# Kernel optimization log

Measured on AMD Instinct MI355X. Metric: run time of the kernel, lower is better.

## Reference

```python
import jax, jax.numpy as jnp
import numpy as np

N_NODES = 100000
N_EDGES = 800000
IN_FEATS = 64
H_FEATS = 64
INTER = 64
NUM_CLASSES = 32
NEG_SLOPE = 0.01  # torch leaky_relu default


def setup_inputs() -> dict:
    key = jax.random.key(0)
    ks = jax.random.split(key, 16)
    inp = {
        "gate_type": jax.random.randint(ks[0], (N_NODES,), 0, IN_FEATS),
        "src": jax.random.randint(ks[1], (N_EDGES,), 0, N_NODES),
        "dst": jax.random.randint(ks[2], (N_EDGES,), 0, N_NODES),
        "src_idx": jax.random.uniform(ks[3], (N_EDGES,), dtype=jnp.float32),
        "dst_idx": jax.random.uniform(ks[4], (N_EDGES,), dtype=jnp.float32),
        "rev": jax.random.uniform(ks[5], (N_EDGES,), dtype=jnp.float32),
        "emb": jax.random.normal(ks[6], (IN_FEATS, IN_FEATS), dtype=jnp.float32) * 0.1,
        # 5 stacked QConv layers (in_feats == h_feats so shapes coincide)
        "W1": jax.random.normal(ks[7], (5, INTER, IN_FEATS + 3), dtype=jnp.float32) * 0.1,
        "W2": jax.random.normal(ks[8], (5, H_FEATS, IN_FEATS + INTER), dtype=jnp.float32) * 0.1,
        "b2": jnp.zeros((5, H_FEATS), dtype=jnp.float32),
        "Wl1": jax.random.normal(ks[9], (H_FEATS, H_FEATS), dtype=jnp.float32) * 0.1,
        "bl1": jnp.zeros((H_FEATS,), dtype=jnp.float32),
        "Wl2": jax.random.normal(ks[10], (NUM_CLASSES, H_FEATS), dtype=jnp.float32) * 0.1,
        "bl2": jnp.zeros((NUM_CLASSES,), dtype=jnp.float32),
    }
    return inp


def _leaky_relu(x):
    return jnp.where(x >= 0, x, NEG_SLOPE * x)


def reference(gate_type, src, dst, src_idx, dst_idx, rev,
              emb, W1, W2, b2, Wl1, bl1, Wl2, bl2):
    n = gate_type.shape[0]
    # edge feature w: [E, 3]
    w = jnp.stack([src_idx, dst_idx, rev], axis=1)
    # in-degree for mailbox mean (zero-degree nodes get h_N = 0, as in DGL)
    deg = jax.ops.segment_sum(jnp.ones((src.shape[0],), w.dtype), dst, num_segments=n)
    inv_deg = (1.0 / jnp.maximum(deg, 1.0))[:, None]  # [N, 1]

    h = emb[gate_type]  # [N, F] embedding lookup
    for i in range(5):
        m = jnp.concatenate([h[src], w], axis=1)          # [E, F+3] gather
        tmp = _leaky_relu(m @ W1[i].T)                     # [E, inter]
        h_N = jax.ops.segment_sum(tmp, dst, num_segments=n) * inv_deg  # mean mailbox
        h = jax.nn.relu(jnp.concatenate([h, h_N], axis=1) @ W2[i].T + b2[i])
    h = jax.nn.relu(h @ Wl1.T + bl1)
    return h @ Wl2.T + bl2  # [N, num_classes]
```

## Files before the change

### kernel.cpp

```cpp
#include <hip/hip_runtime.h>

#define NN 100000
#define NE 800000
#define NBUCK 196
#define EPB 3125
#define BCAP 6144

typedef __attribute__((ext_vector_type(8))) short short8;
typedef __attribute__((ext_vector_type(4))) float f32x4;
typedef unsigned long long u64;

__device__ __forceinline__ unsigned short f2b(float x) {
  unsigned int u = __float_as_uint(x);
  u = u + 0x7fffu + ((u >> 16) & 1u);
  return (unsigned short)(u >> 16);
}
__device__ __forceinline__ float b2f(unsigned short s) {
  return __uint_as_float(((unsigned int)s) << 16);
}

__global__ __launch_bounds__(256) void wprep(
    const float* __restrict__ W1, const float* __restrict__ W2,
    const float* __restrict__ Wl1, const float* __restrict__ Wl2,
    unsigned short* __restrict__ w1p, unsigned short* __restrict__ w2p,
    unsigned short* __restrict__ wl1p, unsigned short* __restrict__ wl2p,
    float* __restrict__ wcolp) {
  int i = blockIdx.x * 256 + threadIdx.x;
  if (i < 20480) {
    int l = i >> 12, r = i & 4095, c = r >> 6, k = r & 63;
    int idx = (((c * 64 + k) * 2) ^ ((c & 7) << 4)) >> 1;
    w1p[l * 4096 + idx] = f2b(W1[(l * 64 + c) * 67 + k]);
  } else if (i < 61440) {
    int j = i - 20480;
    int l = j >> 13, r = j & 8191, c = r >> 7, k = r & 127;
    int idx = (((c * 128 + k) * 2) ^ ((c & 7) << 4)) >> 1;
    w2p[l * 8192 + idx] = f2b(W2[(l * 64 + c) * 128 + k]);
  } else if (i < 65536) {
    int j = i - 61440;
    int c = j >> 6, k = j & 63;
    int idx = (((c * 64 + k) * 2) ^ ((c & 7) << 4)) >> 1;
    wl1p[idx] = f2b(Wl1[c * 64 + k]);
  } else if (i < 67584) {
    int j = i - 65536;
    int c = j >> 6, k = j & 63;
    int idx = (((c * 64 + k) * 2) ^ ((c & 7) << 4)) >> 1;
    wl2p[idx] = f2b(Wl2[c * 64 + k]);
  } else if (i < 68544) {
    int j = i - 67584;
    int l = j / 192, r = j % 192, jj = r >> 6, f = r & 63;
    wcolp[(l * 3 + jj) * 64 + f] = W1[(l * 64 + f) * 67 + 64 + jj];
  }
}


__global__ __launch_bounds__(256) void ehist(const int* __restrict__ dst,
                                             int* __restrict__ hp) {
  __shared__ int lh[NBUCK];
  int tid = threadIdx.x;
  if (tid < NBUCK) lh[tid] = 0;
  __syncthreads();
  int e0 = blockIdx.x * EPB;
  for (int i = tid; i < EPB; i += 256) atomicAdd(&lh[dst[e0 + i] >> 9], 1);
  __syncthreads();
  if (tid < NBUCK) hp[blockIdx.x * NBUCK + tid] = lh[tid];
}

__global__ __launch_bounds__(256) void escatter(
    const int* __restrict__ dst, const int* __restrict__ src,
    const float* __restrict__ si, const float* __restrict__ di,
    const float* __restrict__ rv, const int* __restrict__ hp,
    u64* __restrict__ erec_tmp, unsigned short* __restrict__ lbkt) {
  __shared__ int cur[NBUCK];
  __shared__ int wsum[4];
  int tid = threadIdx.x;
  int myblk = blockIdx.x;
  int tot = 0, mypre = 0;
  if (tid < NBUCK) {
    for (int blk = 0; blk < 256; ++blk) {
      int v = hp[blk * NBUCK + tid];
      tot += v;
      if (blk < myblk) mypre += v;
    }
  }
  int lane = tid & 63, wv = tid >> 6;
  int s = tot;
#pragma unroll
  for (int off = 1; off < 64; off <<= 1) {
    int t = __shfl_up(s, off);
    if (lane >= off) s += t;
  }
  if (lane == 63) wsum[wv] = s;
  __syncthreads();
  int wpre = 0;
  for (int j = 0; j < wv; ++j) wpre += wsum[j];
  int excl = s + wpre - tot;
  if (tid < NBUCK) cur[tid] = excl + mypre;
  __syncthreads();
  int e0 = myblk * EPB;
  for (int i = tid; i < EPB; i += 256) {
    int e = e0 + i;
    int d = dst[e];
    int pos = atomicAdd(&cur[d >> 9], 1);
    unsigned int a = (unsigned int)fminf(si[e] * 32768.f, 32767.f);
    unsigned int b = (unsigned int)fminf(di[e] * 32768.f, 32767.f);
    unsigned int c = (unsigned int)fminf(rv[e] * 32768.f, 32767.f);
    u64 u = (u64)(src[e] & 0x1FFFF) | ((u64)a << 17) | ((u64)b << 32) |
            ((u64)c << 47);
    erec_tmp[pos] = u;
    lbkt[pos] = (unsigned short)(d & 511);
  }
}

__global__ __launch_bounds__(256) void bucket_csr(
    const unsigned short* __restrict__ lbkt, const int* __restrict__ hp,
    const u64* __restrict__ erec_tmp, u64* __restrict__ erec,
    int* __restrict__ deg, float4* __restrict__ meta, int* __restrict__ nhp) {
  __shared__ unsigned short lb[BCAP];
  __shared__ int cnt[512];
  __shared__ int excl[512];
  __shared__ int dh[64];
  __shared__ int wsum[4];
  __shared__ int btot[NBUCK];
  __shared__ int bexcl[NBUCK];
  int b = blockIdx.x, tid = threadIdx.x;
  int tot = 0;
  if (tid < NBUCK) {
    for (int blk = 0; blk < 256; ++blk) tot += hp[blk * NBUCK + tid];
    btot[tid] = tot;
  }
  int lane = tid & 63, wv = tid >> 6;
  int s = tot;
#pragma unroll
  for (int off = 1; off < 64; off <<= 1) {
    int t = __shfl_up(s, off);
    if (lane >= off) s += t;
  }
  if (lane == 63) wsum[wv] = s;
  __syncthreads();
  int wpre = 0;
  for (int j = 0; j < wv; ++j) wpre += wsum[j];
  if (tid < NBUCK) bexcl[tid] = s + wpre - tot;
  cnt[2 * tid] = 0;
  cnt[2 * tid + 1] = 0;
  if (tid < 64) dh[tid] = 0;
  __syncthreads();
  int s0 = bexcl[b];
  int size = btot[b];
  if (size > BCAP) size = BCAP;
  for (int p = tid; p < size; p += 256) {
    unsigned short v = lbkt[s0 + p];
    lb[p] = v;
    atomicAdd(&cnt[v], 1);
  }
  __syncthreads();
  int a = cnt[2 * tid], c = cnt[2 * tid + 1];
  int ps = a + c;
  int v2 = ps;
#pragma unroll
  for (int off = 1; off < 64; off <<= 1) {
    int t = __shfl_up(v2, off);
    if (lane >= off) v2 += t;
  }
  __syncthreads();
  if (lane == 63) wsum[wv] = v2;
  __syncthreads();
  int wpre2 = 0;
  for (int j = 0; j < wv; ++j) wpre2 += wsum[j];
  int ex = v2 + wpre2 - ps;
  excl[2 * tid] = ex;
  excl[2 * tid + 1] = ex + a;
  int n0 = b << 9;
#pragma unroll
  for (int j = 0; j < 2; ++j) {
    int i = 2 * tid + j;
    int n = n0 + i;
    if (n < NN) {
      int d = j ? c : a;
      int rs = s0 + (j ? ex + a : ex);
      deg[n] = d;
      float4 m;
      m.x = __int_as_float(rs);
      m.y = __int_as_float(d);
      m.z = 1.0f / (float)((d > 1) ? d : 1);
      m.w = 0.f;
      meta[n] = m;
      atomicAdd(&dh[(d < 63) ? d : 63], 1);
    }
  }
  cnt[2 * tid] = 0;
  cnt[2 * tid + 1] = 0;
  __syncthreads();
  for (int p = tid; p < size; p += 256) {
    int ld = lb[p];
    int pos = excl[ld] + atomicAdd(&cnt[ld], 1);
    erec[s0 + pos] = erec_tmp[s0 + p];
  }
  if (tid < 64) nhp[b * 64 + tid] = dh[tid];
}

__global__ __launch_bounds__(256) void nscatter(
    const int* __restrict__ deg, const int* __restrict__ nhp,
    int* __restrict__ order) {
  __shared__ int cur[64];
  int tid = threadIdx.x;
  int myblk = blockIdx.x;
  if (tid < 64) {
    int tot = 0, mypre = 0;
    for (int blk = 0; blk < NBUCK; ++blk) {
      int v = nhp[blk * 64 + tid];
      tot += v;
      if (blk < myblk) mypre += v;
    }
    int s = tot;
#pragma unroll
    for (int off = 1; off < 64; off <<= 1) {
      int t = __shfl_up(s, off);
      if (tid >= off) s += t;
    }
    cur[tid] = (s - tot) + mypre;
  }
  __syncthreads();
  int n0 = myblk * 512;
#pragma unroll
  for (int j = 0; j < 2; ++j) {
    int n = n0 + tid + j * 256;
    if (n < NN) {
      int d = deg[n];
      int pos = atomicAdd(&cur[(d < 63) ? d : 63], 1);
      order[pos] = n;
    }
  }
}


__global__ __launch_bounds__(256) void aggregate(
    const unsigned short* __restrict__ H1, const float4* __restrict__ meta,
    const int* __restrict__ order, const u64* __restrict__ erec,
    const float* __restrict__ wcolp, unsigned short* __restrict__ hNs) {
  __shared__ float wcol[3][64];
  int tid = threadIdx.x;
  if (tid < 192) ((float*)wcol)[tid] = wcolp[tid];
  __syncthreads();
  int l = tid & 63;
  int fl = l & 15, f0 = fl * 4;
  int qidx = blockIdx.x * 16 + (tid >> 4);
  float wa[4], wb[4], wc[4];
#pragma unroll
  for (int j = 0; j < 4; ++j) {
    wa[j] = wcol[0][f0 + j];
    wb[j] = wcol[1][f0 + j];
    wc[j] = wcol[2][f0 + j];
  }
  if (qidx >= NN) return;
  int n = order[qidx];
  float4 m = meta[n];
  int s0 = __float_as_int(m.x);
  int cnt = __float_as_int(m.y);
  float invd = m.z;
  float acc[4] = {0.f, 0.f, 0.f, 0.f};
  u64 r0 = 0, r1 = 0, r2 = 0;
  ushort4 h0 = make_ushort4(0, 0, 0, 0), h1 = h0;
  if (cnt > 0) {
    r0 = erec[s0];
    h0 = *(const ushort4*)&H1[(size_t)(r0 & 0x1FFFF) * 64 + f0];
  }
  if (cnt > 1) {
    r1 = erec[s0 + 1];
    h1 = *(const ushort4*)&H1[(size_t)(r1 & 0x1FFFF) * 64 + f0];
  }
  if (cnt > 2) r2 = erec[s0 + 2];
  const float q = 1.f / 32768.f;
  for (int k = 0; k < cnt; ++k) {
    u64 r3 = 0;
    if (k + 3 < cnt) r3 = erec[s0 + k + 3];
    ushort4 h2 = make_ushort4(0, 0, 0, 0);
    if (k + 2 < cnt)
      h2 = *(const ushort4*)&H1[(size_t)(r2 & 0x1FFFF) * 64 + f0];
    float hx[4] = {b2f(h0.x), b2f(h0.y), b2f(h0.z), b2f(h0.w)};
    float si = (float)((unsigned)(r0 >> 17) & 0x7FFF) * q;
    float di = (float)((unsigned)(r0 >> 32) & 0x7FFF) * q;
    float rv = (float)((unsigned)(r0 >> 47) & 0x7FFF) * q;
#pragma unroll
    for (int j = 0; j < 4; ++j) {
      float vv = hx[j] + si * wa[j] + di * wb[j] + rv * wc[j];
      acc[j] += (vv >= 0.f) ? vv : 0.01f * vv;
    }
    r0 = r1;
    r1 = r2;
    r2 = r3;
    h0 = h1;
    h1 = h2;
  }
  ushort4 o = make_ushort4(f2b(acc[0] * invd), f2b(acc[1] * invd),
                           f2b(acc[2] * invd), f2b(acc[3] * invd));
  *(ushort4*)&hNs[(size_t)n * 64 + f0] = o;
}


__device__ __forceinline__ void stageP(const unsigned short* __restrict__ src,
                                       unsigned short* lds, int n, int tid,
                                       int nt) {
  for (int idx = tid; idx * 8 < n; idx += nt)
    *(short8*)&lds[idx * 8] = *(const short8*)&src[idx * 8];
}
__device__ __forceinline__ short8 ldW(const unsigned short* lds, int K, int c,
                                      int k) {
  int byte = (c * K + k) * 2;
  byte ^= ((c & 7) << 4);
  return *(const short8*)((const char*)lds + byte);
}
__device__ __forceinline__ void stH(unsigned short* ht, int row, int col,
                                    unsigned short v) {
  int byte = row * 128 + col * 2;
  byte ^= ((row & 7) << 4);
  *(unsigned short*)((char*)ht + byte) = v;
}
__device__ __forceinline__ short8 ldH(const unsigned short* ht, int row,
                                      int k) {
  int byte = row * 128 + k * 2;
  byte ^= ((row & 7) << 4);
  return *(const short8*)((const char*)ht + byte);
}

__global__ __launch_bounds__(256) void fused0(
    const int* __restrict__ gate, const float* __restrict__ emb,
    const unsigned short* __restrict__ w1p, unsigned short* __restrict__ hout,
    unsigned short* __restrict__ H1out) {
  __shared__ __align__(16) unsigned short W1l[64 * 64];
  int tid = threadIdx.x;
  stageP(w1p, W1l, 64 * 64, tid, 256);
  __syncthreads();
  int w = tid >> 6, l = tid & 63, r16 = l & 15, kg = l >> 4;
  int row_base = blockIdx.x * 128 + w * 32;
  f32x4 acc[2][4];
#pragma unroll
  for (int rt = 0; rt < 2; ++rt)
#pragma unroll
    for (int ct = 0; ct < 4; ++ct) {
      f32x4 z = {0.f, 0.f, 0.f, 0.f};
      acc[rt][ct] = z;
    }
#pragma unroll
  for (int rt = 0; rt < 2; ++rt) {
    int arow = row_base + rt * 16 + r16;
    short8 a0 = {0, 0, 0, 0, 0, 0, 0, 0};
    short8 a1 = {0, 0, 0, 0, 0, 0, 0, 0};
    if (arow < NN) {
      int g = gate[arow];
      const float* ep = &emb[g * 64];
      float4 e0 = *(const float4*)&ep[kg * 8];
      float4 e1 = *(const float4*)&ep[kg * 8 + 4];
      float4 e2 = *(const float4*)&ep[32 + kg * 8];
      float4 e3 = *(const float4*)&ep[32 + kg * 8 + 4];
      a0[0] = (short)f2b(e0.x); a0[1] = (short)f2b(e0.y);
      a0[2] = (short)f2b(e0.z); a0[3] = (short)f2b(e0.w);
      a0[4] = (short)f2b(e1.x); a0[5] = (short)f2b(e1.y);
      a0[6] = (short)f2b(e1.z); a0[7] = (short)f2b(e1.w);
      a1[0] = (short)f2b(e2.x); a1[1] = (short)f2b(e2.y);
      a1[2] = (short)f2b(e2.z); a1[3] = (short)f2b(e2.w);
      a1[4] = (short)f2b(e3.x); a1[5] = (short)f2b(e3.y);
      a1[6] = (short)f2b(e3.z); a1[7] = (short)f2b(e3.w);
      *(short8*)&hout[(size_t)arow * 64 + kg * 8] = a0;
      *(short8*)&hout[(size_t)arow * 64 + 32 + kg * 8] = a1;
    }
#pragma unroll
    for (int ct = 0; ct < 4; ++ct) {
      int c = ct * 16 + r16;
      acc[rt][ct] = __builtin_amdgcn_mfma_f32_16x16x32_bf16(
          a0, ldW(W1l, 64, c, kg * 8), acc[rt][ct], 0, 0, 0);
      acc[rt][ct] = __builtin_amdgcn_mfma_f32_16x16x32_bf16(
          a1, ldW(W1l, 64, c, 32 + kg * 8), acc[rt][ct], 0, 0, 0);
    }
  }
#pragma unroll
  for (int rt = 0; rt < 2; ++rt)
#pragma unroll
    for (int ct = 0; ct < 4; ++ct) {
      int col = ct * 16 + r16;
#pragma unroll
      for (int i = 0; i < 4; ++i) {
        int row = row_base + rt * 16 + kg * 4 + i;
        if (row < NN) H1out[(size_t)row * 64 + col] = f2b(acc[rt][ct][i]);
      }
    }
}

__global__ __launch_bounds__(512) void fused_mid(
    const unsigned short* h, const unsigned short* __restrict__ hNs,
    const unsigned short* __restrict__ w2p, const float* __restrict__ b2,
    const unsigned short* __restrict__ w1np, unsigned short* hout,
    unsigned short* __restrict__ H1out) {
  __shared__ __align__(16) unsigned short W2l[64 * 128];
  __shared__ __align__(16) unsigned short W1l[64 * 64];
  __shared__ __align__(16) unsigned short ht[128 * 64];
  int tid = threadIdx.x;
  stageP(w2p, W2l, 64 * 128, tid, 512);
  stageP(w1np, W1l, 64 * 64, tid, 512);
  __syncthreads();
  int w = tid >> 6, l = tid & 63, r16 = l & 15, kg = l >> 4;
  int row_base = blockIdx.x * 128 + w * 16;
  int arow = row_base + r16;
  short8 z8 = {0, 0, 0, 0, 0, 0, 0, 0};
  short8 a0 = z8, a1 = z8, c0 = z8, c1 = z8;
  if (arow < NN) {
    a0 = *(const short8*)&h[(size_t)arow * 64 + kg * 8];
    a1 = *(const short8*)&h[(size_t)arow * 64 + 32 + kg * 8];
    c0 = *(const short8*)&hNs[(size_t)arow * 64 + kg * 8];
    c1 = *(const short8*)&hNs[(size_t)arow * 64 + 32 + kg * 8];
  }
  f32x4 acc[4];
#pragma unroll
  for (int ct = 0; ct < 4; ++ct) {
    f32x4 z = {0.f, 0.f, 0.f, 0.f};
    acc[ct] = z;
  }
#pragma unroll
  for (int ct = 0; ct < 4; ++ct) {
    int c = ct * 16 + r16;
    acc[ct] = __builtin_amdgcn_mfma_f32_16x16x32_bf16(
        a0, ldW(W2l, 128, c, kg * 8), acc[ct], 0, 0, 0);
    acc[ct] = __builtin_amdgcn_mfma_f32_16x16x32_bf16(
        a1, ldW(W2l, 128, c, 32 + kg * 8), acc[ct], 0, 0, 0);
    acc[ct] = __builtin_amdgcn_mfma_f32_16x16x32_bf16(
        c0, ldW(W2l, 128, c, 64 + kg * 8), acc[ct], 0, 0, 0);
    acc[ct] = __builtin_amdgcn_mfma_f32_16x16x32_bf16(
        c1, ldW(W2l, 128, c, 96 + kg * 8), acc[ct], 0, 0, 0);
  }
#pragma unroll
  for (int ct = 0; ct < 4; ++ct) {
    int col = ct * 16 + r16;
    float bv = b2[col];
#pragma unroll
    for (int i = 0; i < 4; ++i) {
      int lrow = w * 16 + kg * 4 + i;
      float v = acc[ct][i] + bv;
      v = fmaxf(v, 0.f);
      stH(ht, lrow, col, f2b(v));
    }
  }
  __syncthreads();
  f32x4 acc2[4];
#pragma unroll
  for (int ct = 0; ct < 4; ++ct) {
    f32x4 z = {0.f, 0.f, 0.f, 0.f};
    acc2[ct] = z;
  }
  {
    int lrow = w * 16 + r16;
    short8 b0 = ldH(ht, lrow, kg * 8);
    short8 b1 = ldH(ht, lrow, 32 + kg * 8);
    if (arow < NN) {
      *(short8*)&hout[(size_t)arow * 64 + kg * 8] = b0;
      *(short8*)&hout[(size_t)arow * 64 + 32 + kg * 8] = b1;
    }
#pragma unroll
    for (int ct = 0; ct < 4; ++ct) {
      int c = ct * 16 + r16;
      acc2[ct] = __builtin_amdgcn_mfma_f32_16x16x32_bf16(
          b0, ldW(W1l, 64, c, kg * 8), acc2[ct], 0, 0, 0);
      acc2[ct] = __builtin_amdgcn_mfma_f32_16x16x32_bf16(
          b1, ldW(W1l, 64, c, 32 + kg * 8), acc2[ct], 0, 0, 0);
    }
  }
#pragma unroll
  for (int ct = 0; ct < 4; ++ct) {
    int col = ct * 16 + r16;
#pragma unroll
    for (int i = 0; i < 4; ++i) {
      int row = row_base + kg * 4 + i;
      if (row < NN) H1out[(size_t)row * 64 + col] = f2b(acc2[ct][i]);
    }
  }
}

__global__ __launch_bounds__(512) void fused_final(
    const unsigned short* __restrict__ h, const unsigned short* __restrict__ hNs,
    const unsigned short* __restrict__ w2p, const float* __restrict__ b2,
    const unsigned short* __restrict__ wl1p, const float* __restrict__ bl1,
    const unsigned short* __restrict__ wl2p, const float* __restrict__ bl2,
    float* __restrict__ out) {
  __shared__ __align__(16) unsigned short W2l[64 * 128];
  __shared__ __align__(16) unsigned short Al[64 * 64];
  __shared__ __align__(16) unsigned short Bl[32 * 64];
  __shared__ __align__(16) unsigned short ht[128 * 64];
  int tid = threadIdx.x;
  stageP(w2p, W2l, 64 * 128, tid, 512);
  stageP(wl1p, Al, 64 * 64, tid, 512);
  stageP(wl2p, Bl, 32 * 64, tid, 512);
  __syncthreads();
  int w = tid >> 6, l = tid & 63, r16 = l & 15, kg = l >> 4;
  int row_base = blockIdx.x * 128 + w * 16;
  int arow = row_base + r16;
  short8 z8 = {0, 0, 0, 0, 0, 0, 0, 0};
  short8 a0 = z8, a1 = z8, c0 = z8, c1 = z8;
  if (arow < NN) {
    a0 = *(const short8*)&h[(size_t)arow * 64 + kg * 8];
    a1 = *(const short8*)&h[(size_t)arow * 64 + 32 + kg * 8];
    c0 = *(const short8*)&hNs[(size_t)arow * 64 + kg * 8];
    c1 = *(const short8*)&hNs[(size_t)arow * 64 + 32 + kg * 8];
  }
  f32x4 acc[4];
#pragma unroll
  for (int ct = 0; ct < 4; ++ct) {
    f32x4 z = {0.f, 0.f, 0.f, 0.f};
    acc[ct] = z;
  }
#pragma unroll
  for (int ct = 0; ct < 4; ++ct) {
    int c = ct * 16 + r16;
    acc[ct] = __builtin_amdgcn_mfma_f32_16x16x32_bf16(
        a0, ldW(W2l, 128, c, kg * 8), acc[ct], 0, 0, 0);
    acc[ct] = __builtin_amdgcn_mfma_f32_16x16x32_bf16(
        a1, ldW(W2l, 128, c, 32 + kg * 8), acc[ct], 0, 0, 0);
    acc[ct] = __builtin_amdgcn_mfma_f32_16x16x32_bf16(
        c0, ldW(W2l, 128, c, 64 + kg * 8), acc[ct], 0, 0, 0);
    acc[ct] = __builtin_amdgcn_mfma_f32_16x16x32_bf16(
        c1, ldW(W2l, 128, c, 96 + kg * 8), acc[ct], 0, 0, 0);
  }
#pragma unroll
  for (int ct = 0; ct < 4; ++ct) {
    int col = ct * 16 + r16;
    float bv = b2[col];
#pragma unroll
    for (int i = 0; i < 4; ++i) {
      int lrow = w * 16 + kg * 4 + i;
      float v = acc[ct][i] + bv;
      v = fmaxf(v, 0.f);
      stH(ht, lrow, col, f2b(v));
    }
  }
  __syncthreads();
  f32x4 acc2[4];
#pragma unroll
  for (int ct = 0; ct < 4; ++ct) {
    f32x4 z = {0.f, 0.f, 0.f, 0.f};
    acc2[ct] = z;
  }
  {
    int lrow = w * 16 + r16;
    short8 b0 = ldH(ht, lrow, kg * 8);
    short8 b1 = ldH(ht, lrow, 32 + kg * 8);
#pragma unroll
    for (int ct = 0; ct < 4; ++ct) {
      int c = ct * 16 + r16;
      acc2[ct] = __builtin_amdgcn_mfma_f32_16x16x32_bf16(
          b0, ldW(Al, 64, c, kg * 8), acc2[ct], 0, 0, 0);
      acc2[ct] = __builtin_amdgcn_mfma_f32_16x16x32_bf16(
          b1, ldW(Al, 64, c, 32 + kg * 8), acc2[ct], 0, 0, 0);
    }
  }
  __syncthreads();
#pragma unroll
  for (int ct = 0; ct < 4; ++ct) {
    int col = ct * 16 + r16;
    float bv = bl1[col];
#pragma unroll
    for (int i = 0; i < 4; ++i) {
      int lrow = w * 16 + kg * 4 + i;
      float v = acc2[ct][i] + bv;
      v = fmaxf(v, 0.f);
      stH(ht, lrow, col, f2b(v));
    }
  }
  __syncthreads();
  f32x4 acc3[2];
#pragma unroll
  for (int ct = 0; ct < 2; ++ct) {
    f32x4 z = {0.f, 0.f, 0.f, 0.f};
    acc3[ct] = z;
  }
  {
    int lrow = w * 16 + r16;
    short8 b0 = ldH(ht, lrow, kg * 8);
    short8 b1 = ldH(ht, lrow, 32 + kg * 8);
#pragma unroll
    for (int ct = 0; ct < 2; ++ct) {
      int c = ct * 16 + r16;
      acc3[ct] = __builtin_amdgcn_mfma_f32_16x16x32_bf16(
          b0, ldW(Bl, 64, c, kg * 8), acc3[ct], 0, 0, 0);
      acc3[ct] = __builtin_amdgcn_mfma_f32_16x16x32_bf16(
          b1, ldW(Bl, 64, c, 32 + kg * 8), acc3[ct], 0, 0, 0);
    }
  }
#pragma unroll
  for (int ct = 0; ct < 2; ++ct) {
    int col = ct * 16 + r16;
    float bv = bl2[col];
#pragma unroll
    for (int i = 0; i < 4; ++i) {
      int row = row_base + kg * 4 + i;
      if (row < NN) out[(size_t)row * 32 + col] = acc3[ct][i] + bv;
    }
  }
}


extern "C" void kernel_launch(void* const* d_in, const int* in_sizes, int n_in,
                              void* d_out, int out_size, void* d_ws, size_t ws_size,
                              hipStream_t stream) {
  const int* gate = (const int*)d_in[0];
  const int* src = (const int*)d_in[1];
  const int* dst = (const int*)d_in[2];
  const float* src_idx = (const float*)d_in[3];
  const float* dst_idx = (const float*)d_in[4];
  const float* rev = (const float*)d_in[5];
  const float* emb = (const float*)d_in[6];
  const float* W1 = (const float*)d_in[7];
  const float* W2 = (const float*)d_in[8];
  const float* b2 = (const float*)d_in[9];
  const float* Wl1 = (const float*)d_in[10];
  const float* bl1 = (const float*)d_in[11];
  const float* Wl2 = (const float*)d_in[12];
  const float* bl2 = (const float*)d_in[13];
  float* out = (float*)d_out;

  char* ws = (char*)d_ws;
  unsigned short* h = (unsigned short*)(ws + 0);
  unsigned short* lbkt = (unsigned short*)(ws + 0);
  unsigned short* H1 = (unsigned short*)(ws + 12800000);
  unsigned short* hNs = (unsigned short*)(ws + 25600000);
  u64* erec_tmp = (u64*)(ws + 25600000);
  u64* erec = (u64*)(ws + 38400000);
  float4* meta = (float4*)(ws + 51200000);
  int* order = (int*)(ws + 52800000);
  int* deg = (int*)(ws + 53200000);
  int* hp = (int*)(ws + 53600000);
  int* nhp = (int*)(ws + 53820000);
  unsigned short* w1p = (unsigned short*)(ws + 53900000);
  unsigned short* w2p = (unsigned short*)(ws + 53950000);
  unsigned short* wl1p = (unsigned short*)(ws + 54040000);
  unsigned short* wl2p = (unsigned short*)(ws + 54050000);
  float* wcolp = (float*)(ws + 54060000);

  wprep<<<268, 256, 0, stream>>>(W1, W2, Wl1, Wl2, w1p, w2p, wl1p, wl2p, wcolp);
  ehist<<<256, 256, 0, stream>>>(dst, hp);
  escatter<<<256, 256, 0, stream>>>(dst, src, src_idx, dst_idx, rev, hp,
                                    erec_tmp, lbkt);
  bucket_csr<<<NBUCK, 256, 0, stream>>>(lbkt, hp, erec_tmp, erec, deg, meta,
                                        nhp);
  nscatter<<<NBUCK, 256, 0, stream>>>(deg, nhp, order);

  fused0<<<782, 256, 0, stream>>>(gate, emb, w1p, h, H1);
  for (int i = 0; i < 5; ++i) {
    aggregate<<<6250, 256, 0, stream>>>(H1, meta, order, erec, wcolp + i * 192,
                                        hNs);
    if (i < 4)
      fused_mid<<<782, 512, 0, stream>>>(h, hNs, w2p + i * 8192, b2 + i * 64,
                                         w1p + (i + 1) * 4096, h, H1);
  }
  fused_final<<<782, 512, 0, stream>>>(h, hNs, w2p + 4 * 8192, b2 + 4 * 64,
                                       wl1p, bl1, wl2p, bl2, out);
}
```

Measured before the change: 378.5 us.

## Precompute bucket scans once and pack sorted node metadata for aggregation

```diff
diff --git a/kernel.cpp b/kernel.cpp
--- a/kernel.cpp
+++ b/kernel.cpp
@@ -65,38 +65,43 @@
   if (tid < NBUCK) hp[blockIdx.x * NBUCK + tid] = lh[tid];
 }
 
+__global__ void escan(int* __restrict__ hp, int* __restrict__ bucket_start) {
+  __shared__ int wsum[4];
+  int b = threadIdx.x;
+  int running = 0;
+  if (b < NBUCK) {
+    for (int blk = 0; blk < 256; ++blk) {
+      int t = hp[blk * NBUCK + b];
+      hp[blk * NBUCK + b] = running;
+      running += t;
+    }
+  }
+  int lane = b & 63, wv = b >> 6;
+  int v = running;
+#pragma unroll
+  for (int off = 1; off < 64; off <<= 1) {
+    int t = __shfl_up(v, off);
+    if (lane >= off) v += t;
+  }
+  if (lane == 63) wsum[wv] = v;
+  __syncthreads();
+  int wpre = 0;
+  for (int j = 0; j < wv; ++j) wpre += wsum[j];
+  int excl = v + wpre - running;
+  if (b <= NBUCK) bucket_start[b] = excl;
+}
+
 __global__ __launch_bounds__(256) void escatter(
     const int* __restrict__ dst, const int* __restrict__ src,
     const float* __restrict__ si, const float* __restrict__ di,
     const float* __restrict__ rv, const int* __restrict__ hp,
-    u64* __restrict__ erec_tmp, unsigned short* __restrict__ lbkt) {
+    const int* __restrict__ bucket_start, u64* __restrict__ erec_tmp,
+    unsigned short* __restrict__ lbkt) {
   __shared__ int cur[NBUCK];
-  __shared__ int wsum[4];
   int tid = threadIdx.x;
-  int myblk = blockIdx.x;
-  int tot = 0, mypre = 0;
-  if (tid < NBUCK) {
-    for (int blk = 0; blk < 256; ++blk) {
-      int v = hp[blk * NBUCK + tid];
-      tot += v;
-      if (blk < myblk) mypre += v;
-    }
-  }
-  int lane = tid & 63, wv = tid >> 6;
-  int s = tot;
-#pragma unroll
-  for (int off = 1; off < 64; off <<= 1) {
-    int t = __shfl_up(s, off);
-    if (lane >= off) s += t;
-  }
-  if (lane == 63) wsum[wv] = s;
-  __syncthreads();
-  int wpre = 0;
-  for (int j = 0; j < wv; ++j) wpre += wsum[j];
-  int excl = s + wpre - tot;
-  if (tid < NBUCK) cur[tid] = excl + mypre;
-  __syncthreads();
-  int e0 = myblk * EPB;
+  if (tid < NBUCK) cur[tid] = bucket_start[tid] + hp[blockIdx.x * NBUCK + tid];
+  __syncthreads();
+  int e0 = blockIdx.x * EPB;
   for (int i = tid; i < EPB; i += 256) {
     int e = e0 + i;
     int d = dst[e];
@@ -112,41 +117,22 @@
 }
 
 __global__ __launch_bounds__(256) void bucket_csr(
-    const unsigned short* __restrict__ lbkt, const int* __restrict__ hp,
+    const unsigned short* __restrict__ lbkt, const int* __restrict__ bstart,
     const u64* __restrict__ erec_tmp, u64* __restrict__ erec,
-    int* __restrict__ deg, float4* __restrict__ meta, int* __restrict__ nhp) {
+    int* __restrict__ deg, int* __restrict__ rowst, int* __restrict__ nhp) {
   __shared__ unsigned short lb[BCAP];
   __shared__ int cnt[512];
   __shared__ int excl[512];
   __shared__ int dh[64];
   __shared__ int wsum[4];
-  __shared__ int btot[NBUCK];
-  __shared__ int bexcl[NBUCK];
   int b = blockIdx.x, tid = threadIdx.x;
-  int tot = 0;
-  if (tid < NBUCK) {
-    for (int blk = 0; blk < 256; ++blk) tot += hp[blk * NBUCK + tid];
-    btot[tid] = tot;
-  }
-  int lane = tid & 63, wv = tid >> 6;
-  int s = tot;
-#pragma unroll
-  for (int off = 1; off < 64; off <<= 1) {
-    int t = __shfl_up(s, off);
-    if (lane >= off) s += t;
-  }
-  if (lane == 63) wsum[wv] = s;
-  __syncthreads();
-  int wpre = 0;
-  for (int j = 0; j < wv; ++j) wpre += wsum[j];
-  if (tid < NBUCK) bexcl[tid] = s + wpre - tot;
+  int s0 = bstart[b];
+  int size = bstart[b + 1] - s0;
+  if (size > BCAP) size = BCAP;
   cnt[2 * tid] = 0;
   cnt[2 * tid + 1] = 0;
   if (tid < 64) dh[tid] = 0;
   __syncthreads();
-  int s0 = bexcl[b];
-  int size = btot[b];
-  if (size > BCAP) size = BCAP;
   for (int p = tid; p < size; p += 256) {
     unsigned short v = lbkt[s0 + p];
     lb[p] = v;
@@ -155,18 +141,18 @@
   __syncthreads();
   int a = cnt[2 * tid], c = cnt[2 * tid + 1];
   int ps = a + c;
-  int v2 = ps;
+  int lane = tid & 63, wv = tid >> 6;
+  int v = ps;
 #pragma unroll
   for (int off = 1; off < 64; off <<= 1) {
-    int t = __shfl_up(v2, off);
-    if (lane >= off) v2 += t;
-  }
-  __syncthreads();
-  if (lane == 63) wsum[wv] = v2;
-  __syncthreads();
-  int wpre2 = 0;
-  for (int j = 0; j < wv; ++j) wpre2 += wsum[j];
-  int ex = v2 + wpre2 - ps;
+    int t = __shfl_up(v, off);
+    if (lane >= off) v += t;
+  }
+  if (lane == 63) wsum[wv] = v;
+  __syncthreads();
+  int wpre = 0;
+  for (int j = 0; j < wv; ++j) wpre += wsum[j];
+  int ex = v + wpre - ps;
   excl[2 * tid] = ex;
   excl[2 * tid + 1] = ex + a;
   int n0 = b << 9;
@@ -176,14 +162,8 @@
     int n = n0 + i;
     if (n < NN) {
       int d = j ? c : a;
-      int rs = s0 + (j ? ex + a : ex);
       deg[n] = d;
-      float4 m;
-      m.x = __int_as_float(rs);
-      m.y = __int_as_float(d);
-      m.z = 1.0f / (float)((d > 1) ? d : 1);
-      m.w = 0.f;
-      meta[n] = m;
+      rowst[n] = s0 + (j ? ex + a : ex);
       atomicAdd(&dh[(d < 63) ? d : 63], 1);
     }
   }
@@ -198,52 +178,56 @@
   if (tid < 64) nhp[b * 64 + tid] = dh[tid];
 }
 
+__global__ void nscan(int* __restrict__ nhp, int* __restrict__ nbin_start) {
+  int b = threadIdx.x;
+  int running = 0;
+  for (int blk = 0; blk < NBUCK; ++blk) {
+    int t = nhp[blk * 64 + b];
+    nhp[blk * 64 + b] = running;
+    running += t;
+  }
+  int v = running, s = running;
+#pragma unroll
+  for (int off = 1; off < 64; off <<= 1) {
+    int t = __shfl_up(s, off);
+    if (b >= off) s += t;
+  }
+  nbin_start[b] = s - v;
+}
+
 __global__ __launch_bounds__(256) void nscatter(
-    const int* __restrict__ deg, const int* __restrict__ nhp,
-    int* __restrict__ order) {
+    const int* __restrict__ deg, const int* __restrict__ rowst,
+    const int* __restrict__ nhp, const int* __restrict__ nbin_start,
+    u64* __restrict__ smeta) {
   __shared__ int cur[64];
   int tid = threadIdx.x;
-  int myblk = blockIdx.x;
-  if (tid < 64) {
-    int tot = 0, mypre = 0;
-    for (int blk = 0; blk < NBUCK; ++blk) {
-      int v = nhp[blk * 64 + tid];
-      tot += v;
-      if (blk < myblk) mypre += v;
-    }
-    int s = tot;
-#pragma unroll
-    for (int off = 1; off < 64; off <<= 1) {
-      int t = __shfl_up(s, off);
-      if (tid >= off) s += t;
-    }
-    cur[tid] = (s - tot) + mypre;
-  }
-  __syncthreads();
-  int n0 = myblk * 512;
+  if (tid < 64) cur[tid] = nbin_start[tid] + nhp[blockIdx.x * 64 + tid];
+  __syncthreads();
+  int n0 = blockIdx.x * 512;
 #pragma unroll
   for (int j = 0; j < 2; ++j) {
     int n = n0 + tid + j * 256;
     if (n < NN) {
       int d = deg[n];
       int pos = atomicAdd(&cur[(d < 63) ? d : 63], 1);
-      order[pos] = n;
+      smeta[pos] = (u64)(unsigned)rowst[n] | ((u64)(unsigned)d << 20) |
+                   ((u64)(unsigned)n << 30);
     }
   }
 }
 
 
 __global__ __launch_bounds__(256) void aggregate(
-    const unsigned short* __restrict__ H1, const float4* __restrict__ meta,
-    const int* __restrict__ order, const u64* __restrict__ erec,
-    const float* __restrict__ wcolp, unsigned short* __restrict__ hNs) {
+    const unsigned short* __restrict__ H1, const u64* __restrict__ smeta,
+    const u64* __restrict__ erec, const float* __restrict__ wcolp,
+    unsigned short* __restrict__ hNs) {
   __shared__ float wcol[3][64];
   int tid = threadIdx.x;
   if (tid < 192) ((float*)wcol)[tid] = wcolp[tid];
   __syncthreads();
   int l = tid & 63;
   int fl = l & 15, f0 = fl * 4;
-  int qidx = blockIdx.x * 16 + (tid >> 4);
+  int qbase = (blockIdx.x * 16 + (tid >> 4)) * 2;
   float wa[4], wb[4], wc[4];
 #pragma unroll
   for (int j = 0; j < 4; ++j) {
@@ -251,49 +235,53 @@
     wb[j] = wcol[1][f0 + j];
     wc[j] = wcol[2][f0 + j];
   }
-  if (qidx >= NN) return;
-  int n = order[qidx];
-  float4 m = meta[n];
-  int s0 = __float_as_int(m.x);
-  int cnt = __float_as_int(m.y);
-  float invd = m.z;
-  float acc[4] = {0.f, 0.f, 0.f, 0.f};
-  u64 r0 = 0, r1 = 0, r2 = 0;
-  ushort4 h0 = make_ushort4(0, 0, 0, 0), h1 = h0;
-  if (cnt > 0) {
-    r0 = erec[s0];
-    h0 = *(const ushort4*)&H1[(size_t)(r0 & 0x1FFFF) * 64 + f0];
-  }
-  if (cnt > 1) {
-    r1 = erec[s0 + 1];
-    h1 = *(const ushort4*)&H1[(size_t)(r1 & 0x1FFFF) * 64 + f0];
-  }
-  if (cnt > 2) r2 = erec[s0 + 2];
   const float q = 1.f / 32768.f;
-  for (int k = 0; k < cnt; ++k) {
-    u64 r3 = 0;
-    if (k + 3 < cnt) r3 = erec[s0 + k + 3];
-    ushort4 h2 = make_ushort4(0, 0, 0, 0);
-    if (k + 2 < cnt)
-      h2 = *(const ushort4*)&H1[(size_t)(r2 & 0x1FFFF) * 64 + f0];
-    float hx[4] = {b2f(h0.x), b2f(h0.y), b2f(h0.z), b2f(h0.w)};
-    float si = (float)((unsigned)(r0 >> 17) & 0x7FFF) * q;
-    float di = (float)((unsigned)(r0 >> 32) & 0x7FFF) * q;
-    float rv = (float)((unsigned)(r0 >> 47) & 0x7FFF) * q;
-#pragma unroll
-    for (int j = 0; j < 4; ++j) {
-      float vv = hx[j] + si * wa[j] + di * wb[j] + rv * wc[j];
-      acc[j] += (vv >= 0.f) ? vv : 0.01f * vv;
-    }
-    r0 = r1;
-    r1 = r2;
-    r2 = r3;
-    h0 = h1;
-    h1 = h2;
-  }
-  ushort4 o = make_ushort4(f2b(acc[0] * invd), f2b(acc[1] * invd),
-                           f2b(acc[2] * invd), f2b(acc[3] * invd));
-  *(ushort4*)&hNs[(size_t)n * 64 + f0] = o;
+#pragma unroll 1
+  for (int t = 0; t < 2; ++t) {
+    int qidx = qbase + t;
+    if (qidx >= NN) return;
+    u64 sm = smeta[qidx];
+    int s0 = (int)(sm & 0xFFFFF);
+    int cnt = (int)((sm >> 20) & 0x3FF);
+    int n = (int)(sm >> 30);
+    float invd = 1.f / fmaxf((float)cnt, 1.f);
+    float acc[4] = {0.f, 0.f, 0.f, 0.f};
+    u64 r0 = 0, r1 = 0, r2 = 0;
+    ushort4 h0 = make_ushort4(0, 0, 0, 0), h1 = h0;
+    if (cnt > 0) {
+      r0 = erec[s0];
+      h0 = *(const ushort4*)&H1[(size_t)(r0 & 0x1FFFF) * 64 + f0];
+    }
+    if (cnt > 1) {
+      r1 = erec[s0 + 1];
+      h1 = *(const ushort4*)&H1[(size_t)(r1 & 0x1FFFF) * 64 + f0];
+    }
+    if (cnt > 2) r2 = erec[s0 + 2];
+    for (int k = 0; k < cnt; ++k) {
+      u64 r3 = 0;
+      if (k + 3 < cnt) r3 = erec[s0 + k + 3];
+      ushort4 h2 = make_ushort4(0, 0, 0, 0);
+      if (k + 2 < cnt)
+        h2 = *(const ushort4*)&H1[(size_t)(r2 & 0x1FFFF) * 64 + f0];
+      float hx[4] = {b2f(h0.x), b2f(h0.y), b2f(h0.z), b2f(h0.w)};
+      float si = (float)((unsigned)(r0 >> 17) & 0x7FFF) * q;
+      float di = (float)((unsigned)(r0 >> 32) & 0x7FFF) * q;
+      float rv = (float)((unsigned)(r0 >> 47) & 0x7FFF) * q;
+#pragma unroll
+      for (int j = 0; j < 4; ++j) {
+        float vv = hx[j] + si * wa[j] + di * wb[j] + rv * wc[j];
+        acc[j] += (vv >= 0.f) ? vv : 0.01f * vv;
+      }
+      r0 = r1;
+      r1 = r2;
+      r2 = r3;
+      h0 = h1;
+      h1 = h2;
+    }
+    ushort4 o = make_ushort4(f2b(acc[0] * invd), f2b(acc[1] * invd),
+                             f2b(acc[2] * invd), f2b(acc[3] * invd));
+    *(ushort4*)&hNs[(size_t)n * 64 + f0] = o;
+  }
 }
 
 
@@ -621,11 +609,13 @@
   unsigned short* hNs = (unsigned short*)(ws + 25600000);
   u64* erec_tmp = (u64*)(ws + 25600000);
   u64* erec = (u64*)(ws + 38400000);
-  float4* meta = (float4*)(ws + 51200000);
-  int* order = (int*)(ws + 52800000);
+  u64* smeta = (u64*)(ws + 51200000);
+  int* rowst = (int*)(ws + 52800000);
   int* deg = (int*)(ws + 53200000);
   int* hp = (int*)(ws + 53600000);
+  int* bucket_start = (int*)(ws + 53810000);
   int* nhp = (int*)(ws + 53820000);
+  int* nbin_start = (int*)(ws + 53880000);
   unsigned short* w1p = (unsigned short*)(ws + 53900000);
   unsigned short* w2p = (unsigned short*)(ws + 53950000);
   unsigned short* wl1p = (unsigned short*)(ws + 54040000);
@@ -634,16 +624,17 @@
 
   wprep<<<268, 256, 0, stream>>>(W1, W2, Wl1, Wl2, w1p, w2p, wl1p, wl2p, wcolp);
   ehist<<<256, 256, 0, stream>>>(dst, hp);
+  escan<<<1, 256, 0, stream>>>(hp, bucket_start);
   escatter<<<256, 256, 0, stream>>>(dst, src, src_idx, dst_idx, rev, hp,
-                                    erec_tmp, lbkt);
-  bucket_csr<<<NBUCK, 256, 0, stream>>>(lbkt, hp, erec_tmp, erec, deg, meta,
-                                        nhp);
-  nscatter<<<NBUCK, 256, 0, stream>>>(deg, nhp, order);
+                                    bucket_start, erec_tmp, lbkt);
+  bucket_csr<<<NBUCK, 256, 0, stream>>>(lbkt, bucket_start, erec_tmp, erec,
+                                        deg, rowst, nhp);
+  nscan<<<1, 64, 0, stream>>>(nhp, nbin_start);
+  nscatter<<<NBUCK, 256, 0, stream>>>(deg, rowst, nhp, nbin_start, smeta);
 
   fused0<<<782, 256, 0, stream>>>(gate, emb, w1p, h, H1);
   for (int i = 0; i < 5; ++i) {
-    aggregate<<<6250, 256, 0, stream>>>(H1, meta, order, erec, wcolp + i * 192,
-                                        hNs);
+    aggregate<<<3125, 256, 0, stream>>>(H1, smeta, erec, wcolp + i * 192, hNs);
     if (i < 4)
       fused_mid<<<782, 512, 0, stream>>>(h, hNs, w2p + i * 8192, b2 + i * 64,
                                          w1p + (i + 1) * 4096, h, H1);
```

Measured after the change: 392.2 us. 1.04x slower.
